# Optimization experiments

Measured on AMD Instinct MI355X. Metric: run time of the kernel, lower is better.

## Reference

```python
import jax, jax.numpy as jnp
import numpy as np

B, S, D, H = 2, 2048, 768, 12
DK = D // H


def setup_inputs() -> dict:
    key = jax.random.key(0)
    ks = jax.random.split(key, 10)
    sc = 0.02
    return {
        "k": jax.random.normal(ks[0], (B, S, D), jnp.float32),
        "q": jax.random.normal(ks[1], (B, S, D), jnp.float32),
        "v": jax.random.normal(ks[2], (B, S, D), jnp.float32),
        "mask": jnp.ones((B, 1, S, S), jnp.int32),
        "wq": jax.random.normal(ks[3], (D, D), jnp.float32) * sc,
        "bq": jnp.zeros((D,), jnp.float32),
        "wk": jax.random.normal(ks[4], (D, D), jnp.float32) * sc,
        "bk": jnp.zeros((D,), jnp.float32),
        "wv": jax.random.normal(ks[5], (D, D), jnp.float32) * sc,
        "bv": jnp.zeros((D,), jnp.float32),
        "wo": jax.random.normal(ks[6], (D, D), jnp.float32) * sc,
        "bo": jnp.zeros((D,), jnp.float32),
    }


def reference(k, q, v, mask, wq, bq, wk, bk, wv, bv, wo, bo):
    # Linear projections (torch Linear: x @ W^T + b)
    query = q @ wq.T + bq
    key_ = k @ wk.T + bk
    value = v @ wv.T + bv
    # [B,S,D] -> [B,H,S,DK]
    def split_heads(x):
        return x.reshape(B, S, H, DK).transpose(0, 2, 1, 3)
    Q, K, V = split_heads(query), split_heads(key_), split_heads(value)
    # NOTE: original masked_fill result is discarded -> mask is a no-op.
    scores = jnp.einsum("bhqd,bhkd->bhqk", Q, K) / jnp.sqrt(jnp.float32(DK))
    attn = jax.nn.softmax(scores, axis=-1)  # dropout p=0.0 -> identity
    out = jnp.einsum("bhqk,bhkd->bhqd", attn, V)
    out = out.transpose(0, 2, 1, 3).reshape(B, S, D)
    return out @ wo.T + bo
```

## Files before the change

### kernel.cpp

```cpp
#include <hip/hip_runtime.h>
#include <hip/hip_bf16.h>

#define B_  2
#define S_  2048
#define D_  768
#define H_  12
#define DK_ 64
#define NX_ (B_*S_*D_)
#define NW_ (D_*D_)
#define CSC 0.18033688011112042f

typedef __attribute__((ext_vector_type(8))) short  bf16x8;
typedef __attribute__((ext_vector_type(4))) float  f32x4;

__device__ __forceinline__ unsigned short f2bf(float f) {
    unsigned int u = __float_as_uint(f);
    u += 0x7fffu + ((u >> 16) & 1u);
    return (unsigned short)(u >> 16);
}

__device__ __forceinline__ unsigned pack_bf2(float a, float b) {
    const unsigned ua = __float_as_uint(a) + 0x8000u;
    const unsigned ub = __float_as_uint(b) + 0x8000u;
    return __builtin_amdgcn_perm(ub, ua, 0x07060302u);
}

__device__ __forceinline__ void async_cp16(const unsigned short* g,
                                           const unsigned short* lds_uniform_base) {
    __builtin_amdgcn_global_load_lds(
        (const __attribute__((address_space(1))) unsigned int*)(uintptr_t)g,
        (__attribute__((address_space(3))) unsigned int*)(unsigned int)(uintptr_t)lds_uniform_base,
        16, 0, 0);
}

struct CvtArgs { const float* s[7]; };

__global__ __launch_bounds__(256) void cvt_all(CvtArgs a,
                                               unsigned short* __restrict__ Xsw,
                                               unsigned short* __restrict__ Wsw) {
    const int bx = blockIdx.x;
    int y, inner;
    if (bx < 2304) { y = bx / 768;             inner = bx % 768; }
    else           { y = 3 + (bx - 2304) / 144; inner = (bx - 2304) % 144; }
    const int idx = inner * 256 + threadIdx.x;
    const int n  = idx / 48;
    const int g2 = idx % 48;
    const float* src = a.s[y] + (long)n * D_ + g2 * 16;
    const float zs = (y == 3) ? CSC : 1.0f;
    unsigned short o[16];
#pragma unroll
    for (int i = 0; i < 4; i++) {
        const float4 f = *(const float4*)(src + i * 4);
        o[i*4+0] = f2bf(f.x*zs); o[i*4+1] = f2bf(f.y*zs);
        o[i*4+2] = f2bf(f.z*zs); o[i*4+3] = f2bf(f.w*zs);
    }
    unsigned short* dst = (y >= 3) ? (Wsw + (long)(y - 3) * NW_ + (long)n * D_)
                                   : (Xsw + (long)y * NX_ + (long)n * D_);
    const int key = n & 7;
#pragma unroll
    for (int h = 0; h < 2; h++) {
        const int g8 = g2 * 2 + h;
        const int kdst = (g8 >> 3) * 64 + (((g8 & 7) ^ key) * 8);
        *(uint4*)(dst + kdst) = *(const uint4*)&o[h * 8];
    }
}

struct QkvArgs { const float* bias[3]; unsigned short* out[3]; };

__global__ __launch_bounds__(256, 3) void gemm_qkv(QkvArgs args,
                                                   const unsigned short* __restrict__ Xsw,
                                                   const unsigned short* __restrict__ Wsw) {
    __shared__ __align__(16) unsigned short smem[17408];
    unsigned short* As = smem;
    unsigned short* Bs = smem + 8192;

    const int t    = threadIdx.x;
    const int wave = t >> 6;
    const int lane = t & 63;
    const int l16  = lane & 15;
    const int quad = lane >> 4;
    const int wm   = wave >> 1, wn = wave & 1;
    const int m0   = blockIdx.x * 128;
    const int zz   = blockIdx.y / 6;
    const int nb   = blockIdx.y % 6;
    const int n0   = nb * 128;

    const unsigned short* Ap = Xsw + (long)zz * NX_;
    const unsigned short* Wp = Wsw + (long)zz * NW_;

    f32x4 acc[4][4];
#pragma unroll
    for (int s = 0; s < 4; s++)
#pragma unroll
        for (int j = 0; j < 4; j++) acc[s][j] = (f32x4){0.f, 0.f, 0.f, 0.f};

    const int lrow = lane >> 3;
    const int lcg  = lane & 7;

    for (int k0 = 0; k0 < D_; k0 += 64) {
        __syncthreads();
#pragma unroll
        for (int i = 0; i < 4; i++) {
            const int chunk = wave * 4 + i;
            async_cp16(Ap + (long)(m0 + chunk * 8 + lrow) * D_ + k0 + lcg * 8,
                       As + chunk * 512);
        }
#pragma unroll
        for (int i = 0; i < 4; i++) {
            const int chunk = wave * 4 + i;
            async_cp16(Wp + (long)(n0 + chunk * 8 + lrow) * D_ + k0 + lcg * 8,
                       Bs + chunk * 512);
        }
        __syncthreads();
#pragma unroll
        for (int ks = 0; ks < 2; ks++) {
            const int cg = ks * 4 + quad;
            bf16x8 af[4], bf[4];
#pragma unroll
            for (int s = 0; s < 4; s++) {
                const int r = wm * 64 + s * 16 + l16;
                af[s] = *(const bf16x8*)&As[r * 64 + ((cg ^ (r & 7)) * 8)];
            }
#pragma unroll
            for (int j = 0; j < 4; j++) {
                const int r = wn * 64 + j * 16 + l16;
                bf[j] = *(const bf16x8*)&Bs[r * 64 + ((cg ^ (r & 7)) * 8)];
            }
#pragma unroll
            for (int s = 0; s < 4; s++)
#pragma unroll
                for (int j = 0; j < 4; j++)
                    acc[s][j] = __builtin_amdgcn_mfma_f32_16x16x32_bf16(af[s], bf[j], acc[s][j], 0, 0, 0);
        }
    }
    __syncthreads();

    const int b     = m0 >> 11;
    const int sbase = m0 & (S_ - 1);
    const float zs  = (zz == 0) ? CSC : 1.0f;
    float bv[4];
#pragma unroll
    for (int j = 0; j < 4; j++) bv[j] = args.bias[zz][n0 + wn * 64 + j * 16 + l16] * zs;

    if (zz < 2) {
        unsigned short* Ls = smem;
#pragma unroll
        for (int s = 0; s < 4; s++)
#pragma unroll
            for (int j = 0; j < 4; j++)
#pragma unroll
                for (int r = 0; r < 4; r++)
                    Ls[(wm * 64 + s * 16 + quad * 4 + r) * 136 + wn * 64 + j * 16 + l16] =
                        f2bf(acc[s][j][r] + bv[j]);
        __syncthreads();
        const int row  = t >> 1;
        const int half = t & 1;
        unsigned short* Op = args.out[zz];
#pragma unroll
        for (int i = 0; i < 8; i++) {
            const int col  = half * 64 + i * 8;
            const int head = nb * 2 + half;
            const uint4 v = *(const uint4*)&Ls[row * 136 + col];
            *(uint4*)(Op + ((long)(b * H_ + head) * S_ + sbase + row) * DK_ + (col & 63)) = v;
        }
    } else {
        unsigned short* Ls = smem;
#pragma unroll
        for (int s = 0; s < 4; s++)
#pragma unroll
            for (int j = 0; j < 4; j++)
#pragma unroll
                for (int r = 0; r < 4; r++) {
                    const int dk  = j * 16 + l16;
                    const int pos = wm * 64 + (quad * 4 + r) * 4 + s;
                    Ls[wn * 8704 + dk * 136 + pos] = f2bf(acc[s][j][r] + bv[j]);
                }
        __syncthreads();
        const int rowIdx = t >> 1;
        const int hh = rowIdx >> 6, dk = rowIdx & 63;
        const int half = t & 1;
        unsigned short* Op = args.out[2];
#pragma unroll
        for (int i = 0; i < 8; i++) {
            const int col = half * 64 + i * 8;
            const uint4 v = *(const uint4*)&Ls[hh * 8704 + dk * 136 + col];
            const int head = nb * 2 + hh;
            *(uint4*)(Op + ((long)(b * H_ + head) * DK_ + dk) * S_ + sbase + col) = v;
        }
    }
}

__global__ __launch_bounds__(256, 3) void attn_kernel(
    const unsigned short* __restrict__ Q, const unsigned short* __restrict__ K,
    const unsigned short* __restrict__ Vt, unsigned short* __restrict__ Ao)
{
    const int t    = threadIdx.x;
    const int wave = t >> 6;
    const int lane = t & 63;
    const int l16  = lane & 15;
    const int quad = lane >> 4;
    const int qtile = blockIdx.x;
    const int bh    = blockIdx.y;

    const unsigned short* Qp = Q  + (long)bh * S_ * DK_;
    const unsigned short* Kp = K  + (long)bh * S_ * DK_;
    const unsigned short* Vp = Vt + (long)bh * DK_ * S_;

    __shared__ __align__(16) unsigned short smem[23040];
    unsigned short* Ps = smem + 18432;

    bf16x8 qfrag[2];
    {
        const long qoff = (long)(qtile * 64 + wave * 16 + l16) * DK_ + quad * 8;
        qfrag[0] = *(const bf16x8*)(Qp + qoff);
        qfrag[1] = *(const bf16x8*)(Qp + qoff + 32);
    }

    const int srow = t >> 2;
    const int scg  = (t & 3) * 16;
    uint4 kreg[2], vreg[2];
    const unsigned short* gk = Kp + (long)srow * DK_ + scg;
    const unsigned short* gv = Vp + (long)srow * S_ + scg;
    kreg[0] = *(const uint4*)gk;  kreg[1] = *(const uint4*)(gk + 8);
    vreg[0] = *(const uint4*)gv;  vreg[1] = *(const uint4*)(gv + 8);
    gk += 64 * DK_;  gv += 64;
    *(uint4*)&smem[srow * 72 + scg]            = kreg[0];
    *(uint4*)&smem[srow * 72 + scg + 8]        = kreg[1];
    *(uint4*)&smem[9216 + srow * 72 + scg]     = vreg[0];
    *(uint4*)&smem[9216 + srow * 72 + scg + 8] = vreg[1];

    f32x4 oacc[4];
#pragma unroll
    for (int j = 0; j < 4; j++) oacc[j] = (f32x4){0.f, 0.f, 0.f, 0.f};
    float lsum[4] = {0.f, 0.f, 0.f, 0.f};

    for (int it = 0; it < 32; ++it) {
        const int co = (it & 1) * 4608;
        const int no = ((it & 1) ^ 1) * 4608;
        __syncthreads();
        const unsigned short* Ks = smem + co;
        const unsigned short* Vs = smem + 9216 + co;

        if (it < 31) {
            kreg[0] = *(const uint4*)gk;  kreg[1] = *(const uint4*)(gk + 8);
            vreg[0] = *(const uint4*)gv;  vreg[1] = *(const uint4*)(gv + 8);
            gk += 64 * DK_;  gv += 64;
        }

        f32x4 sacc[4];
#pragma unroll
        for (int j = 0; j < 4; j++) sacc[j] = (f32x4){0.f, 0.f, 0.f, 0.f};
#pragma unroll
        for (int ks = 0; ks < 2; ks++)
#pragma unroll
            for (int j = 0; j < 4; j++) {
                const bf16x8 bf = *(const bf16x8*)&Ks[(j * 16 + l16) * 72 + ks * 32 + quad * 8];
                sacc[j] = __builtin_amdgcn_mfma_f32_16x16x32_bf16(qfrag[ks], bf, sacc[j], 0, 0, 0);
            }

#pragma unroll
        for (int r = 0; r < 4; r++) {
            const float p0 = exp2f(sacc[0][r]);
            const float p1 = exp2f(sacc[1][r]);
            const float p2 = exp2f(sacc[2][r]);
            const float p3 = exp2f(sacc[3][r]);
            lsum[r] += (p0 + p1) + (p2 + p3);
            uint2 pk = {pack_bf2(p0, p1), pack_bf2(p2, p3)};
            *(uint2*)&Ps[(wave * 16 + quad * 4 + r) * 72 + l16 * 4] = pk;
        }

#pragma unroll
        for (int ks = 0; ks < 2; ks++) {
            const bf16x8 pf = *(const bf16x8*)&Ps[(wave * 16 + l16) * 72 + ks * 32 + quad * 8];
#pragma unroll
            for (int j = 0; j < 4; j++) {
                const bf16x8 vf = *(const bf16x8*)&Vs[(j * 16 + l16) * 72 + ks * 32 + quad * 8];
                oacc[j] = __builtin_amdgcn_mfma_f32_16x16x32_bf16(pf, vf, oacc[j], 0, 0, 0);
            }
        }

        if (it < 31) {
            *(uint4*)&smem[no + srow * 72 + scg]            = kreg[0];
            *(uint4*)&smem[no + srow * 72 + scg + 8]        = kreg[1];
            *(uint4*)&smem[9216 + no + srow * 72 + scg]     = vreg[0];
            *(uint4*)&smem[9216 + no + srow * 72 + scg + 8] = vreg[1];
        }
    }

#pragma unroll
    for (int r = 0; r < 4; r++) {
#pragma unroll
        for (int off = 1; off < 16; off <<= 1)
            lsum[r] += __shfl_xor(lsum[r], off, 64);
        lsum[r] = 1.f / lsum[r];
    }

    __syncthreads();
#pragma unroll
    for (int j = 0; j < 4; j++)
#pragma unroll
        for (int r = 0; r < 4; r++)
            Ps[(wave * 16 + quad * 4 + r) * 72 + j * 16 + l16] =
                f2bf(oacc[j][r] * lsum[r]);

    const int b = bh / H_, h = bh % H_;
    const int row = t >> 2;
    const int c0  = (t & 3) * 16;
    const int qrow = qtile * 64 + row;
    const int key  = qrow & 7;
    const uint4 v0 = *(const uint4*)&Ps[row * 72 + c0];
    const uint4 v1 = *(const uint4*)&Ps[row * 72 + c0 + 8];
    const int g8 = c0 >> 3;
    unsigned short* dst = Ao + (long)(b * S_ + qrow) * D_ + h * DK_;
    *(uint4*)(dst + ((g8 ^ key) * 8))       = v0;
    *(uint4*)(dst + (((g8 + 1) ^ key) * 8)) = v1;
}

__global__ __launch_bounds__(256, 4) void gemm_out(
    const unsigned short* __restrict__ A, const unsigned short* __restrict__ Wsw,
    const float* __restrict__ bias, float* __restrict__ Out)
{
    __shared__ __align__(16) unsigned short smem[8704];
    unsigned short* As = smem;
    unsigned short* Bs = smem + 4096;

    const int t    = threadIdx.x;
    const int wave = t >> 6;
    const int lane = t & 63;
    const int l16  = lane & 15;
    const int quad = lane >> 4;
    const int wm   = wave >> 1, wn = wave & 1;
    const int m0   = blockIdx.x * 64;
    const int n0   = blockIdx.y * 64;

    f32x4 acc[2][2];
#pragma unroll
    for (int s = 0; s < 2; s++)
#pragma unroll
        for (int j = 0; j < 2; j++) acc[s][j] = (f32x4){0.f, 0.f, 0.f, 0.f};

    const int lrow = lane >> 3;
    const int lcg  = lane & 7;

    for (int k0 = 0; k0 < D_; k0 += 64) {
        __syncthreads();
#pragma unroll
        for (int i = 0; i < 2; i++) {
            const int chunk = wave * 2 + i;
            async_cp16(A + (long)(m0 + chunk * 8 + lrow) * D_ + k0 + lcg * 8,
                       As + chunk * 512);
        }
#pragma unroll
        for (int i = 0; i < 2; i++) {
            const int chunk = wave * 2 + i;
            async_cp16(Wsw + (long)(n0 + chunk * 8 + lrow) * D_ + k0 + lcg * 8,
                       Bs + chunk * 512);
        }
        __syncthreads();
#pragma unroll
        for (int ks = 0; ks < 2; ks++) {
            const int cg = ks * 4 + quad;
            bf16x8 af[2], bf[2];
#pragma unroll
            for (int s = 0; s < 2; s++) {
                const int r = wm * 32 + s * 16 + l16;
                af[s] = *(const bf16x8*)&As[r * 64 + ((cg ^ (r & 7)) * 8)];
            }
#pragma unroll
            for (int j = 0; j < 2; j++) {
                const int r = wn * 32 + j * 16 + l16;
                bf[j] = *(const bf16x8*)&Bs[r * 64 + ((cg ^ (r & 7)) * 8)];
            }
#pragma unroll
            for (int s = 0; s < 2; s++)
#pragma unroll
                for (int j = 0; j < 2; j++)
                    acc[s][j] = __builtin_amdgcn_mfma_f32_16x16x32_bf16(af[s], bf[j], acc[s][j], 0, 0, 0);
        }
    }

    float bv[2];
#pragma unroll
    for (int j = 0; j < 2; j++) bv[j] = bias[n0 + wn * 32 + j * 16 + l16];

    __syncthreads();
    float* fl = (float*)smem;
#pragma unroll
    for (int s = 0; s < 2; s++)
#pragma unroll
        for (int j = 0; j < 2; j++)
#pragma unroll
            for (int r = 0; r < 4; r++)
                fl[(wm * 32 + s * 16 + quad * 4 + r) * 67 + wn * 32 + j * 16 + l16] =
                    acc[s][j][r] + bv[j];
    __syncthreads();
    const int row = t >> 2, c0 = (t & 3) * 16;
#pragma unroll
    for (int i = 0; i < 4; i++) {
        const float4 v = *(const float4*)&fl[row * 67 + c0 + i * 4];
        *(float4*)(Out + (long)(m0 + row) * D_ + n0 + c0 + i * 4) = v;
    }
}

extern "C" void kernel_launch(void* const* d_in, const int* in_sizes, int n_in,
                              void* d_out, int out_size, void* d_ws, size_t ws_size,
                              hipStream_t stream) {
    const float* k_in = (const float*)d_in[0];
    const float* q_in = (const float*)d_in[1];
    const float* v_in = (const float*)d_in[2];
    const float* wq = (const float*)d_in[4];
    const float* bq = (const float*)d_in[5];
    const float* wk = (const float*)d_in[6];
    const float* bk = (const float*)d_in[7];
    const float* wv = (const float*)d_in[8];
    const float* bv = (const float*)d_in[9];
    const float* wo = (const float*)d_in[10];
    const float* bo = (const float*)d_in[11];

    unsigned short* ws = (unsigned short*)d_ws;
    unsigned short* Wsw = ws;
    unsigned short* Qb  = Wsw + 4ll * NW_;
    unsigned short* Kb  = Qb + (long)NX_;
    unsigned short* Vt  = Kb + (long)NX_;
    unsigned short* Xsw = Vt + (long)NX_;
    unsigned short* Ao  = Xsw;

    CvtArgs ca;
    ca.s[0] = q_in; ca.s[1] = k_in; ca.s[2] = v_in;
    ca.s[3] = wq;   ca.s[4] = wk;   ca.s[5] = wv;  ca.s[6] = wo;
    cvt_all<<<dim3(2880), 256, 0, stream>>>(ca, Xsw, Wsw);

    QkvArgs qa;
    qa.bias[0] = bq; qa.bias[1] = bk; qa.bias[2] = bv;
    qa.out[0] = Qb;  qa.out[1] = Kb;  qa.out[2] = Vt;
    gemm_qkv<<<dim3(32, 18), 256, 0, stream>>>(qa, Xsw, Wsw);

    attn_kernel<<<dim3(S_ / 64, B_ * H_), 256, 0, stream>>>(Qb, Kb, Vt, Ao);

    gemm_out<<<dim3(64, 12), 256, 0, stream>>>(Ao, Wsw + 3ll * NW_, bo, (float*)d_out);
}
```

Baseline: 213.3 us.

## Rewrite attention inner loop with 32x32x16 MFMA and register-resident P

The attention kernel switches from 16x16x32 to 32x32x16 bf16 MFMA. Scores are computed transposed (K as the A operand) so the exponentiated probabilities can be packed with v_cvt_pk_bf16_f32 and v_permlane32_swap and fed straight into the PV MFMA, with no LDS round trip for P. The four waves split into 2 query halves by 2 key halves, and the partial O accumulators and row sums are reduced through LDS at the end. The V-transpose store order in the projection kernel is changed to match the new V fragment layout. This removes P stores and loads and their bank traffic, at the cost of an extra cross-wave reduction and more accumulator registers.

```diff
diff --git a/kernel.cpp b/kernel.cpp
--- a/kernel.cpp
+++ b/kernel.cpp
@@ -12,6 +12,7 @@
 
 typedef __attribute__((ext_vector_type(8))) short  bf16x8;
 typedef __attribute__((ext_vector_type(4))) float  f32x4;
+typedef __attribute__((ext_vector_type(16))) float f32x16;
 
 __device__ __forceinline__ unsigned short f2bf(float f) {
     unsigned int u = __float_as_uint(f);
@@ -19,10 +20,14 @@
     return (unsigned short)(u >> 16);
 }
 
-__device__ __forceinline__ unsigned pack_bf2(float a, float b) {
-    const unsigned ua = __float_as_uint(a) + 0x8000u;
-    const unsigned ub = __float_as_uint(b) + 0x8000u;
-    return __builtin_amdgcn_perm(ub, ua, 0x07060302u);
+__device__ __forceinline__ unsigned cvtpk(float a, float b) {
+    unsigned r;
+    asm("v_cvt_pk_bf16_f32 %0, %1, %2" : "=v"(r) : "v"(a), "v"(b));
+    return r;
+}
+
+__device__ __forceinline__ void plswap(unsigned &a, unsigned &b) {
+    asm("v_permlane32_swap_b32 %0, %1" : "+v"(a), "+v"(b));
 }
 
 __device__ __forceinline__ void async_cp16(const unsigned short* g,
@@ -172,7 +177,7 @@
 #pragma unroll
                 for (int r = 0; r < 4; r++) {
                     const int dk  = j * 16 + l16;
-                    const int pos = wm * 64 + (quad * 4 + r) * 4 + s;
+                    const int pos = wm * 64 + s * 16 + quad * 4 + r;
                     Ls[wn * 8704 + dk * 136 + pos] = f2bf(acc[s][j][r] + bv[j]);
                 }
         __syncthreads();
@@ -197,8 +202,10 @@
     const int t    = threadIdx.x;
     const int wave = t >> 6;
     const int lane = t & 63;
-    const int l16  = lane & 15;
-    const int quad = lane >> 4;
+    const int l31  = lane & 31;
+    const int hi   = lane >> 5;
+    const int wq   = wave & 1;
+    const int wk   = wave >> 1;
     const int qtile = blockIdx.x;
     const int bh    = blockIdx.y;
 
@@ -206,40 +213,41 @@
     const unsigned short* Kp = K  + (long)bh * S_ * DK_;
     const unsigned short* Vp = Vt + (long)bh * DK_ * S_;
 
-    __shared__ __align__(16) unsigned short smem[23040];
-    unsigned short* Ps = smem + 18432;
-
-    bf16x8 qfrag[2];
+    __shared__ __align__(16) unsigned short smem[17408];
+
+    bf16x8 qf[4];
     {
-        const long qoff = (long)(qtile * 64 + wave * 16 + l16) * DK_ + quad * 8;
-        qfrag[0] = *(const bf16x8*)(Qp + qoff);
-        qfrag[1] = *(const bf16x8*)(Qp + qoff + 32);
-    }
-
-    const int srow = t >> 2;
-    const int scg  = (t & 3) * 16;
+        const long qbase = (long)(qtile * 64 + wq * 32 + l31) * DK_ + hi * 8;
+#pragma unroll
+        for (int ks = 0; ks < 4; ks++)
+            qf[ks] = *(const bf16x8*)(Qp + qbase + ks * 16);
+    }
+
+    const int so = (t >> 2) * 68 + (t & 3) * 16;
+    const unsigned short* gk = Kp + (t >> 2) * DK_ + (t & 3) * 16;
+    const unsigned short* gv = Vp + (long)(t >> 2) * S_ + (t & 3) * 16;
     uint4 kreg[2], vreg[2];
-    const unsigned short* gk = Kp + (long)srow * DK_ + scg;
-    const unsigned short* gv = Vp + (long)srow * S_ + scg;
     kreg[0] = *(const uint4*)gk;  kreg[1] = *(const uint4*)(gk + 8);
     vreg[0] = *(const uint4*)gv;  vreg[1] = *(const uint4*)(gv + 8);
     gk += 64 * DK_;  gv += 64;
-    *(uint4*)&smem[srow * 72 + scg]            = kreg[0];
-    *(uint4*)&smem[srow * 72 + scg + 8]        = kreg[1];
-    *(uint4*)&smem[9216 + srow * 72 + scg]     = vreg[0];
-    *(uint4*)&smem[9216 + srow * 72 + scg + 8] = vreg[1];
-
-    f32x4 oacc[4];
-#pragma unroll
-    for (int j = 0; j < 4; j++) oacc[j] = (f32x4){0.f, 0.f, 0.f, 0.f};
-    float lsum[4] = {0.f, 0.f, 0.f, 0.f};
+    *(uint4*)&smem[so]            = kreg[0];
+    *(uint4*)&smem[so + 8]        = kreg[1];
+    *(uint4*)&smem[8704 + so]     = vreg[0];
+    *(uint4*)&smem[8704 + so + 8] = vreg[1];
+
+    f32x16 oacc[2];
+#pragma unroll
+    for (int jb = 0; jb < 2; jb++)
+#pragma unroll
+        for (int i = 0; i < 16; i++) oacc[jb][i] = 0.f;
+    float lsum = 0.f;
 
     for (int it = 0; it < 32; ++it) {
-        const int co = (it & 1) * 4608;
-        const int no = ((it & 1) ^ 1) * 4608;
+        const int co = (it & 1) * 4352;
+        const int no = 4352 - co;
         __syncthreads();
         const unsigned short* Ks = smem + co;
-        const unsigned short* Vs = smem + 9216 + co;
+        const unsigned short* Vs = smem + 8704 + co;
 
         if (it < 31) {
             kreg[0] = *(const uint4*)gk;  kreg[1] = *(const uint4*)(gk + 8);
@@ -247,73 +255,106 @@
             gk += 64 * DK_;  gv += 64;
         }
 
-        f32x4 sacc[4];
-#pragma unroll
-        for (int j = 0; j < 4; j++) sacc[j] = (f32x4){0.f, 0.f, 0.f, 0.f};
-#pragma unroll
-        for (int ks = 0; ks < 2; ks++)
-#pragma unroll
-            for (int j = 0; j < 4; j++) {
-                const bf16x8 bf = *(const bf16x8*)&Ks[(j * 16 + l16) * 72 + ks * 32 + quad * 8];
-                sacc[j] = __builtin_amdgcn_mfma_f32_16x16x32_bf16(qfrag[ks], bf, sacc[j], 0, 0, 0);
-            }
-
-#pragma unroll
-        for (int r = 0; r < 4; r++) {
-            const float p0 = exp2f(sacc[0][r]);
-            const float p1 = exp2f(sacc[1][r]);
-            const float p2 = exp2f(sacc[2][r]);
-            const float p3 = exp2f(sacc[3][r]);
-            lsum[r] += (p0 + p1) + (p2 + p3);
-            uint2 pk = {pack_bf2(p0, p1), pack_bf2(p2, p3)};
-            *(uint2*)&Ps[(wave * 16 + quad * 4 + r) * 72 + l16 * 4] = pk;
-        }
-
-#pragma unroll
-        for (int ks = 0; ks < 2; ks++) {
-            const bf16x8 pf = *(const bf16x8*)&Ps[(wave * 16 + l16) * 72 + ks * 32 + quad * 8];
-#pragma unroll
-            for (int j = 0; j < 4; j++) {
-                const bf16x8 vf = *(const bf16x8*)&Vs[(j * 16 + l16) * 72 + ks * 32 + quad * 8];
-                oacc[j] = __builtin_amdgcn_mfma_f32_16x16x32_bf16(pf, vf, oacc[j], 0, 0, 0);
+        f32x16 sacc;
+#pragma unroll
+        for (int i = 0; i < 16; i++) sacc[i] = 0.f;
+#pragma unroll
+        for (int ks = 0; ks < 4; ks++) {
+            const bf16x8 kf = *(const bf16x8*)&Ks[(wk * 32 + l31) * 68 + ks * 16 + hi * 8];
+            sacc = __builtin_amdgcn_mfma_f32_32x32x16_bf16(kf, qf[ks], sacc, 0, 0, 0);
+        }
+
+        float p[16];
+#pragma unroll
+        for (int r = 0; r < 16; r++) p[r] = exp2f(sacc[r]);
+        {
+            const float s0 = (p[0] + p[1]) + (p[2] + p[3]);
+            const float s1 = (p[4] + p[5]) + (p[6] + p[7]);
+            const float s2 = (p[8] + p[9]) + (p[10] + p[11]);
+            const float s3 = (p[12] + p[13]) + (p[14] + p[15]);
+            lsum += (s0 + s1) + (s2 + s3);
+        }
+
+        unsigned a0 = cvtpk(p[0],  p[1]),  a1 = cvtpk(p[2],  p[3]);
+        unsigned b0 = cvtpk(p[4],  p[5]),  b1 = cvtpk(p[6],  p[7]);
+        unsigned c0 = cvtpk(p[8],  p[9]),  c1 = cvtpk(p[10], p[11]);
+        unsigned d0 = cvtpk(p[12], p[13]), d1 = cvtpk(p[14], p[15]);
+        plswap(a0, b0);  plswap(a1, b1);
+        plswap(c0, d0);  plswap(c1, d1);
+        uint4 pq0 = {a0, a1, b0, b1};
+        uint4 pq1 = {c0, c1, d0, d1};
+        const bf16x8 pa0 = *(const bf16x8*)&pq0;
+        const bf16x8 pa1 = *(const bf16x8*)&pq1;
+
+#pragma unroll
+        for (int ks2 = 0; ks2 < 2; ks2++) {
+            const bf16x8 pf = ks2 ? pa1 : pa0;
+#pragma unroll
+            for (int jb = 0; jb < 2; jb++) {
+                const bf16x8 vf = *(const bf16x8*)&Vs[(jb * 32 + l31) * 68 + wk * 32 + ks2 * 16 + hi * 8];
+                oacc[jb] = __builtin_amdgcn_mfma_f32_32x32x16_bf16(pf, vf, oacc[jb], 0, 0, 0);
             }
         }
 
         if (it < 31) {
-            *(uint4*)&smem[no + srow * 72 + scg]            = kreg[0];
-            *(uint4*)&smem[no + srow * 72 + scg + 8]        = kreg[1];
-            *(uint4*)&smem[9216 + no + srow * 72 + scg]     = vreg[0];
-            *(uint4*)&smem[9216 + no + srow * 72 + scg + 8] = vreg[1];
-        }
-    }
-
-#pragma unroll
-    for (int r = 0; r < 4; r++) {
-#pragma unroll
-        for (int off = 1; off < 16; off <<= 1)
-            lsum[r] += __shfl_xor(lsum[r], off, 64);
-        lsum[r] = 1.f / lsum[r];
-    }
-
+            *(uint4*)&smem[no + so]            = kreg[0];
+            *(uint4*)&smem[no + so + 8]        = kreg[1];
+            *(uint4*)&smem[8704 + no + so]     = vreg[0];
+            *(uint4*)&smem[8704 + no + so + 8] = vreg[1];
+        }
+    }
+
+    lsum += __shfl_xor(lsum, 32, 64);
     __syncthreads();
-#pragma unroll
-    for (int j = 0; j < 4; j++)
-#pragma unroll
-        for (int r = 0; r < 4; r++)
-            Ps[(wave * 16 + quad * 4 + r) * 72 + j * 16 + l16] =
-                f2bf(oacc[j][r] * lsum[r]);
-
-    const int b = bh / H_, h = bh % H_;
-    const int row = t >> 2;
-    const int c0  = (t & 3) * 16;
-    const int qrow = qtile * 64 + row;
-    const int key  = qrow & 7;
-    const uint4 v0 = *(const uint4*)&Ps[row * 72 + c0];
-    const uint4 v1 = *(const uint4*)&Ps[row * 72 + c0 + 8];
-    const int g8 = c0 >> 3;
-    unsigned short* dst = Ao + (long)(b * S_ + qrow) * D_ + h * DK_;
-    *(uint4*)(dst + ((g8 ^ key) * 8))       = v0;
-    *(uint4*)(dst + (((g8 + 1) ^ key) * 8)) = v1;
+    float* LoF = (float*)smem;
+    float* Ll  = (float*)(smem + 8192);
+
+    if (wk == 1) {
+#pragma unroll
+        for (int jb = 0; jb < 2; jb++)
+#pragma unroll
+            for (int r = 0; r < 16; r++) {
+                const int qloc = (r & 3) + 8 * (r >> 2) + 4 * hi;
+                LoF[(wq * 32 + qloc) * 64 + jb * 32 + l31] = oacc[jb][r];
+            }
+        Ll[wq * 32 + l31] = lsum;
+    }
+    __syncthreads();
+    if (wk == 0) {
+#pragma unroll
+        for (int jb = 0; jb < 2; jb++)
+#pragma unroll
+            for (int r = 0; r < 16; r++) {
+                const int qloc = (r & 3) + 8 * (r >> 2) + 4 * hi;
+                oacc[jb][r] += LoF[(wq * 32 + qloc) * 64 + jb * 32 + l31];
+            }
+        const float inv = 1.f / (lsum + Ll[wq * 32 + l31]);
+        float scl[16];
+#pragma unroll
+        for (int r = 0; r < 16; r++)
+            scl[r] = __shfl(inv, (r & 3) + 8 * (r >> 2) + 4 * hi, 64);
+
+        unsigned short* scr = smem + 8704 + wq * 2304;
+#pragma unroll
+        for (int jb = 0; jb < 2; jb++)
+#pragma unroll
+            for (int r = 0; r < 16; r++) {
+                const int qloc = (r & 3) + 8 * (r >> 2) + 4 * hi;
+                scr[qloc * 72 + jb * 32 + l31] = f2bf(oacc[jb][r] * scl[r]);
+            }
+        const int row  = lane >> 1;
+        const int half = lane & 1;
+        const int qrow = qtile * 64 + wq * 32 + row;
+        const int key  = qrow & 7;
+        const int b = bh / H_, h = bh % H_;
+        unsigned short* dst = Ao + (long)(b * S_ + qrow) * D_ + h * DK_;
+#pragma unroll
+        for (int i = 0; i < 4; i++) {
+            const int g8 = half * 4 + i;
+            const uint4 v = *(const uint4*)&scr[row * 72 + half * 32 + i * 8];
+            *(uint4*)(dst + ((g8 ^ key) * 8)) = v;
+        }
+    }
 }
 
 __global__ __launch_bounds__(256, 4) void gemm_out(
```

Measured after the change: 263.8 us. +23.6%, slower.
